# Kernel tuning notes

Measured on AMD Instinct MI355X. Metric: run time of the kernel, lower is better.

The kernel has to match this reference:

```python
import jax, jax.numpy as jnp
import numpy as np
from jax import lax

KSIZE = 5  # covariance window size

def _avg_pool_same(x):
    # TF avg_pool2d with SAME padding: zero-pad sums, divide by count of VALID (non-pad) elems
    win = (1, KSIZE, KSIZE, 1)
    s = lax.reduce_window(x, 0.0, lax.add, win, (1, 1, 1, 1), 'SAME')
    cnt = lax.reduce_window(jnp.ones((1, x.shape[1], x.shape[2], 1), x.dtype), 0.0, lax.add, win, (1, 1, 1, 1), 'SAME')
    return s / cnt

def _detect_plane_xz(xyz):
    B, H, W, _ = xyz.shape
    P = _avg_pool_same(xyz)                                   # [B,H,W,3] windowed mean
    xyz2 = (xyz[..., :, None] * xyz[..., None, :]).reshape(B, H, W, 9)
    S = _avg_pool_same(xyz2).reshape(B, H, W, 3, 3)            # windowed second moment
    A = S - P[..., :, None] * P[..., None, :]                  # covariance sigma
    A_max = jnp.max(jnp.abs(A), axis=(-2, -1))
    eval_zero = (A_max < 1e-6).astype(xyz.dtype)
    A = A / jnp.maximum(A_max[..., None, None], 1e-6)
    a00, a11, a22 = A[..., 0, 0], A[..., 1, 1], A[..., 2, 2]
    a01, a02, a12 = A[..., 0, 1], A[..., 0, 2], A[..., 1, 2]
    norm = a01 ** 2 + a02 ** 2 + a12 ** 2
    q = (a00 + a11 + a22) / 3.0
    b00, b11, b22 = a00 - q, a11 - q, a22 - q
    p = jnp.sqrt((b00 ** 2 + b11 ** 2 + b22 ** 2 + 2.0 * norm) / 6.0)
    eig_triple = (p < 1e-6).astype(xyz.dtype) * (1.0 - eval_zero)
    c00 = b11 * b22 - a12 * a12
    c01 = a01 * b22 - a12 * a02
    c02 = a01 * a12 - b11 * a02
    det = (b00 * c00 - a01 * c01 + a02 * c02) / jnp.maximum(p, 1e-6) ** 3
    half_det = jnp.clip(0.5 * det, -1.0, 1.0)
    angle = jnp.arccos(half_det) / 3.0
    beta2 = jnp.cos(angle) * 2.0
    beta0 = jnp.cos(angle + np.pi * 2.0 / 3.0) * 2.0
    beta1 = -(beta0 + beta2)
    betas = jnp.stack([beta0, beta1, beta2], axis=-1)
    evals = q[..., None] + p[..., None] * betas
    evals = (eig_triple * q)[..., None] + ((1.0 - eval_zero) * (1.0 - eig_triple))[..., None] * evals
    eval0, eval1, eval2 = evals[..., 0], evals[..., 1], evals[..., 2]
    denom = jnp.sqrt(jnp.maximum((eval0 - eval1) * (eval0 - eval2), 0.0))
    evec_zero = (denom < 1e-6).astype(xyz.dtype)
    ny_num = jnp.sqrt(jnp.maximum(eval0 ** 2 - (a00 + a22) * eval0 + (a00 * a22 - a02 ** 2), 0.0))
    ny = jnp.clip(ny_num / jnp.maximum(denom, 1e-6), 0.0, 1.0)
    return (1.0 - evec_zero) * ny

def _populate_pcd(depth, K):
    B, H, W, _ = depth.shape
    px, py = jnp.meshgrid(jnp.arange(W, dtype=depth.dtype), jnp.arange(H, dtype=depth.dtype))
    grid = jnp.stack([px, py, jnp.ones_like(px)], axis=-1)   # [H,W,3] homogeneous pixels
    xyz = grid[None] * depth                                 # [B,H,W,3]
    K_inv = jnp.linalg.inv(K)
    return jnp.einsum('bij,bhwj->bhwi', K_inv, xyz)

def setup_inputs():
    key = jax.random.key(0)
    B, H, W = 8, 384, 1280
    disp = jax.random.uniform(key, (B, H, W, 1), jnp.float32, 0.005, 0.3)  # normalized disparity
    K0 = jnp.tile(jnp.array([[720.0, 0.0, W / 2.0], [0.0, 720.0, H / 2.0], [0.0, 0.0, 1.0]], jnp.float32)[None], (B, 1, 1))
    baseline = 0.54 * jnp.ones((B,), jnp.float32)
    return {"disp": disp, "K0": K0, "baseline": baseline, "h0": H, "w0": W}

def reference(disp, K0, baseline, h0, w0):
    B, h1, w1, _ = disp.shape
    rw = float(w1) / float(w0)
    rh = float(h1) / float(h0)
    K_scale = jnp.array([[rw, 0.0, 0.5 * (rw - 1.0)], [0.0, rh, 0.5 * (rh - 1.0)], [0.0, 0.0, 1.0]], jnp.float32)
    K1 = K_scale[None] @ K0
    fxb = K1[:, 0, 0] * baseline
    d = float(w1) * jnp.maximum(disp, 1e-6)
    depth = fxb[:, None, None, None] / d
    xyz = _populate_pcd(depth, K1)
    plane_xz = _detect_plane_xz(xyz)
    cond1 = (xyz[..., 1] > 0.3).astype(jnp.float32)
    cond2 = (plane_xz > 0.85).astype(jnp.float32)
    return depth, cond1 * cond2
```

## Files before the change

kernel.cpp:

```cpp
#include <hip/hip_runtime.h>

#define BATCH 8
#define HH 384
#define WW 1280
#define TW 32
#define TH 8
#define NT (TW * TH)
#define LW (TW + 4)
#define LH (TH + 4)

__device__ __forceinline__ float fast_rcp(float x) {
  float r = __builtin_amdgcn_rcpf(x);
  return fmaf(r, fmaf(-x, r, 1.0f), r);
}
__device__ __forceinline__ float fast_sqrt(float x) {
  return __builtin_amdgcn_sqrtf(x);
}
__device__ __forceinline__ float cos_rev(float r) {
  float d;
  asm("v_cos_f32 %0, %1" : "=v"(d) : "v"(r));
  return d;
}
__device__ __forceinline__ float fast_acos(float x) {
  const float ax = fabsf(x);
  const bool big = ax > 0.5f;
  const float z = big ? (1.0f - ax) * 0.5f : x * x;
  const float u = big ? fast_sqrt(z) : x;
  float pz = fmaf(z, 4.2163199048e-2f, 2.4181311049e-2f);
  pz = fmaf(z, pz, 4.5470025998e-2f);
  pz = fmaf(z, pz, 7.4953002686e-2f);
  pz = fmaf(z, pz, 1.6666752422e-1f);
  const float r = fmaf(u * z, pz, u);
  const float big_res = (x < 0.0f) ? fmaf(-2.0f, r, 3.14159265358979f) : 2.0f * r;
  const float small_res = 1.57079632679490f - r;
  return big ? big_res : small_res;
}

__global__ void prep_kernel(const float* __restrict__ K0,
                            const float* __restrict__ baseline,
                            const int* __restrict__ h0p,
                            const int* __restrict__ w0p,
                            float* __restrict__ cst) {
  int b = threadIdx.x;
  if (b >= BATCH) return;
  float w0 = (float)w0p[0];
  float h0 = (float)h0p[0];
  float rw = (float)WW / w0;
  float rh = (float)HH / h0;
  float s02 = 0.5f * (rw - 1.0f);
  float s12 = 0.5f * (rh - 1.0f);
  const float* K = K0 + b * 9;
  float k0 = rw * K[0] + s02 * K[6];
  float k1 = rw * K[1] + s02 * K[7];
  float k2 = rw * K[2] + s02 * K[8];
  float k3 = rh * K[3] + s12 * K[6];
  float k4 = rh * K[4] + s12 * K[7];
  float k5 = rh * K[5] + s12 * K[8];
  float k6 = K[6], k7 = K[7], k8 = K[8];
  double a = k0, bb = k1, c = k2, d = k3, e = k4, f = k5, g = k6, h = k7, i = k8;
  double cA = e * i - f * h;
  double cB = -(d * i - f * g);
  double cC = d * h - e * g;
  double det = a * cA + bb * cB + c * cC;
  double idet = 1.0 / det;
  float* o = cst + b * 12;
  o[0] = (float)(cA * idet);
  o[1] = (float)(-(bb * i - c * h) * idet);
  o[2] = (float)((bb * f - c * e) * idet);
  o[3] = (float)(cB * idet);
  o[4] = (float)((a * i - c * g) * idet);
  o[5] = (float)(-(a * f - c * d) * idet);
  o[6] = (float)(cC * idet);
  o[7] = (float)(-(a * h - bb * g) * idet);
  o[8] = (float)((a * e - bb * d) * idet);
  o[9] = k0 * baseline[b];
}

__global__ __launch_bounds__(256) void tmap_fused(
    const float* __restrict__ disp,
    const float* __restrict__ cst,
    float* __restrict__ out_depth,
    float* __restrict__ out_mask) {
  __shared__ float4 tile[LH][LW];
  __shared__ float4 vs0[TH][LW];
  __shared__ float4 vs1[TH][LW];
  __shared__ float  vs2[TH][LW];

  const int b = blockIdx.z;
  const float* C = cst + b * 12;
  const float Ki00 = C[0], Ki01 = C[1], Ki02 = C[2];
  const float Ki10 = C[3], Ki11 = C[4], Ki12 = C[5];
  const float Ki20 = C[6], Ki21 = C[7], Ki22 = C[8];
  const float fxb = C[9];

  const int j0 = blockIdx.x * TW;
  const int i0 = blockIdx.y * TH;
  const int tid = threadIdx.y * TW + threadIdx.x;

  for (int s = tid; s < LH * LW; s += NT) {
    const int ti = s / LW;
    const int tj = s - ti * LW;
    const int gi = i0 - 2 + ti;
    const int gj = j0 - 2 + tj;
    float4 v = make_float4(0.0f, 0.0f, 0.0f, 0.0f);
    if (gi >= 0 && gi < HH && gj >= 0 && gj < WW) {
      const float dsp = disp[(b * HH + gi) * WW + gj];
      const float dd = (float)WW * fmaxf(dsp, 1e-6f);
      const float depth = fxb * fast_rcp(dd);
      const float jf = (float)gj;
      const float iff = (float)gi;
      v.x = depth * fmaf(Ki00, jf, fmaf(Ki01, iff, Ki02));
      v.y = depth * fmaf(Ki10, jf, fmaf(Ki11, iff, Ki12));
      v.z = depth * fmaf(Ki20, jf, fmaf(Ki21, iff, Ki22));
      v.w = depth;
    }
    tile[ti][tj] = v;
  }
  __syncthreads();

  for (int s = tid; s < TH * LW; s += NT) {
    const int ti = s / LW;
    const int tj = s - ti * LW;
    float sx = 0.f, sy = 0.f, sz = 0.f;
    float sxx = 0.f, sxy = 0.f, sxz = 0.f, syy = 0.f, syz = 0.f, szz = 0.f;
#pragma unroll
    for (int k = 0; k < 5; ++k) {
      const float4 v = tile[ti + k][tj];
      sx += v.x; sy += v.y; sz += v.z;
      sxx = fmaf(v.x, v.x, sxx);
      sxy = fmaf(v.x, v.y, sxy);
      sxz = fmaf(v.x, v.z, sxz);
      syy = fmaf(v.y, v.y, syy);
      syz = fmaf(v.y, v.z, syz);
      szz = fmaf(v.z, v.z, szz);
    }
    vs0[ti][tj] = make_float4(sx, sy, sz, sxx);
    vs1[ti][tj] = make_float4(sxy, sxz, syy, syz);
    vs2[ti][tj] = szz;
  }
  __syncthreads();

  float s1x = 0.f, s1y = 0.f, s1z = 0.f;
  float m00 = 0.f, m01 = 0.f, m02 = 0.f, m11 = 0.f, m12 = 0.f, m22 = 0.f;
#pragma unroll
  for (int w = 0; w < 5; ++w) {
    const float4 va = vs0[threadIdx.y][threadIdx.x + w];
    const float4 vb = vs1[threadIdx.y][threadIdx.x + w];
    const float vc = vs2[threadIdx.y][threadIdx.x + w];
    s1x += va.x; s1y += va.y; s1z += va.z; m00 += va.w;
    m01 += vb.x; m02 += vb.y; m11 += vb.z; m12 += vb.w;
    m22 += vc;
  }

  const int gi = i0 + threadIdx.y;
  const int gj = j0 + threadIdx.x;
  const int ch = min(gi + 2, HH - 1) - max(gi - 2, 0) + 1;
  const int cw = min(gj + 2, WW - 1) - max(gj - 2, 0) + 1;
  const float cnt = (float)(ch * cw);
  const float rcnt = fast_rcp(cnt);

  const float Px = s1x * rcnt, Py = s1y * rcnt, Pz = s1z * rcnt;
  float a00 = m00 * rcnt - Px * Px;
  float a01 = m01 * rcnt - Px * Py;
  float a02 = m02 * rcnt - Px * Pz;
  float a11 = m11 * rcnt - Py * Py;
  float a12 = m12 * rcnt - Py * Pz;
  float a22 = m22 * rcnt - Pz * Pz;

  const float AmA = fmaxf(fmaxf(fabsf(a00), fabsf(a11)), fabsf(a22));
  const float AmB = fmaxf(fmaxf(fabsf(a01), fabsf(a02)), fabsf(a12));
  const float Amax = fmaxf(AmA, AmB);
  const float eval_zero = (Amax < 1e-6f) ? 1.0f : 0.0f;
  const float rAm = fast_rcp(fmaxf(Amax, 1e-6f));
  a00 *= rAm; a01 *= rAm; a02 *= rAm; a11 *= rAm; a12 *= rAm; a22 *= rAm;

  const float nrm = a01 * a01 + a02 * a02 + a12 * a12;
  const float q = (a00 + a11 + a22) * (1.0f / 3.0f);
  const float b00 = a00 - q, b11 = a11 - q, b22 = a22 - q;
  const float p =
      fast_sqrt((b00 * b00 + b11 * b11 + b22 * b22 + 2.0f * nrm) * (1.0f / 6.0f));
  const float eig_triple = ((p < 1e-6f) ? 1.0f : 0.0f) * (1.0f - eval_zero);
  const float c00 = b11 * b22 - a12 * a12;
  const float c01 = a01 * b22 - a12 * a02;
  const float c02 = a01 * a12 - b11 * a02;
  const float rpm = fast_rcp(fmaxf(p, 1e-6f));
  const float det = (b00 * c00 - a01 * c01 + a02 * c02) * (rpm * rpm * rpm);
  const float half_det = fminf(fmaxf(0.5f * det, -1.0f), 1.0f);
  const float t = fast_acos(half_det);
  const float rev = t * 0.05305164769729845f;
  const float beta2 = 2.0f * cos_rev(rev);
  const float beta0 = 2.0f * cos_rev(rev + (1.0f / 3.0f));
  const float wsel = (1.0f - eval_zero) * (1.0f - eig_triple);
  const float e0 = eig_triple * q + wsel * fmaf(p, beta0, q);
  const float dd2 = (2.0f * beta0 + beta2) * (beta0 - beta2);
  const float denom = wsel * p * fast_sqrt(fmaxf(dd2, 0.0f));
  const float evec_zero = (denom < 1e-6f) ? 1.0f : 0.0f;
  const float ny_num =
      fast_sqrt(fmaxf(e0 * e0 - (a00 + a22) * e0 + (a00 * a22 - a02 * a02), 0.0f));
  const float ny =
      fminf(fmaxf(ny_num * fast_rcp(fmaxf(denom, 1e-6f)), 0.0f), 1.0f);
  const float plane_xz = (1.0f - evec_zero) * ny;

  const float4 ctr = tile[threadIdx.y + 2][threadIdx.x + 2];
  const float cond1 = (ctr.y > 0.3f) ? 1.0f : 0.0f;
  const float cond2 = (plane_xz > 0.85f) ? 1.0f : 0.0f;

  const int idx = (b * HH + gi) * WW + gj;
  out_depth[idx] = ctr.w;
  out_mask[idx] = cond1 * cond2;
}

extern "C" void kernel_launch(void* const* d_in, const int* in_sizes, int n_in,
                              void* d_out, int out_size, void* d_ws, size_t ws_size,
                              hipStream_t stream) {
  const float* disp = (const float*)d_in[0];
  const float* K0 = (const float*)d_in[1];
  const float* baseline = (const float*)d_in[2];
  const int* h0 = (const int*)d_in[3];
  const int* w0 = (const int*)d_in[4];

  float* cst = (float*)d_ws;
  float* out_depth = (float*)d_out;
  float* out_mask = out_depth + (size_t)BATCH * HH * WW;

  prep_kernel<<<1, BATCH, 0, stream>>>(K0, baseline, h0, w0, cst);

  dim3 block(TW, TH);
  dim3 grid(WW / TW, HH / TH, BATCH);
  tmap_fused<<<grid, block, 0, stream>>>(disp, cst, out_depth, out_mask);
}
```

Measured before the change: 116.9 us.

## Restructure into per-wavefront column strips with register-rolling vertical window

Each wavefront now owns a 64-column strip (60 outputs plus halo) and walks down 8 rows. The five-row vertical sums of the moments are kept in a rolling register buffer, and the horizontal pass goes through per-wave LDS with only wave barriers instead of block-wide syncthreads. This removes the large shared xyz tile, the separate vertical-sum pass and the block synchronisation. In exchange, 4 of 64 lanes do redundant eigen math and register pressure rises. Depth output is taken from z, which equals depth only when the inverse intrinsic's last row is [0,0,1].

```diff
diff --git a/kernel.cpp b/kernel.cpp
--- a/kernel.cpp
+++ b/kernel.cpp
@@ -3,11 +3,10 @@
 #define BATCH 8
 #define HH 384
 #define WW 1280
-#define TW 32
-#define TH 8
-#define NT (TW * TH)
-#define LW (TW + 4)
-#define LH (TH + 4)
+#define OUTW 60
+#define CH 8
+#define NSX 22
+#define NCY 48
 
 __device__ __forceinline__ float fast_rcp(float x) {
   float r = __builtin_amdgcn_rcpf(x);
@@ -76,138 +75,164 @@
   o[9] = k0 * baseline[b];
 }
 
-__global__ __launch_bounds__(256) void tmap_fused(
+__global__ __launch_bounds__(256, 4) void tmap_fused(
     const float* __restrict__ disp,
     const float* __restrict__ cst,
     float* __restrict__ out_depth,
     float* __restrict__ out_mask) {
-  __shared__ float4 tile[LH][LW];
-  __shared__ float4 vs0[TH][LW];
-  __shared__ float4 vs1[TH][LW];
-  __shared__ float  vs2[TH][LW];
-
-  const int b = blockIdx.z;
+  __shared__ float4 S0[4][64];
+  __shared__ float4 S1[4][64];
+  __shared__ float  S2[4][64];
+
+  const int lane = threadIdx.x;
+  const int wv = threadIdx.y;
+  const int unit = blockIdx.x * 4 + wv;
+  const int b = unit / (NSX * NCY);
+  const int rem = unit - b * (NSX * NCY);
+  const int cy = rem / NSX;
+  const int sx = rem - cy * NSX;
+  const int gj0 = sx * OUTW;
+  const int gi0 = cy * CH;
+
   const float* C = cst + b * 12;
-  const float Ki00 = C[0], Ki01 = C[1], Ki02 = C[2];
-  const float Ki10 = C[3], Ki11 = C[4], Ki12 = C[5];
-  const float Ki20 = C[6], Ki21 = C[7], Ki22 = C[8];
+  const float Ki01 = C[1], Ki11 = C[4], Ki21 = C[7];
   const float fxb = C[9];
 
-  const int j0 = blockIdx.x * TW;
-  const int i0 = blockIdx.y * TH;
-  const int tid = threadIdx.y * TW + threadIdx.x;
-
-  for (int s = tid; s < LH * LW; s += NT) {
-    const int ti = s / LW;
-    const int tj = s - ti * LW;
-    const int gi = i0 - 2 + ti;
-    const int gj = j0 - 2 + tj;
-    float4 v = make_float4(0.0f, 0.0f, 0.0f, 0.0f);
-    if (gi >= 0 && gi < HH && gj >= 0 && gj < WW) {
-      const float dsp = disp[(b * HH + gi) * WW + gj];
-      const float dd = (float)WW * fmaxf(dsp, 1e-6f);
-      const float depth = fxb * fast_rcp(dd);
-      const float jf = (float)gj;
-      const float iff = (float)gi;
-      v.x = depth * fmaf(Ki00, jf, fmaf(Ki01, iff, Ki02));
-      v.y = depth * fmaf(Ki10, jf, fmaf(Ki11, iff, Ki12));
-      v.z = depth * fmaf(Ki20, jf, fmaf(Ki21, iff, Ki22));
-      v.w = depth;
+  const int cj = gj0 + lane - 2;
+  const bool colv = ((unsigned)cj < (unsigned)WW);
+  const float jf = (float)cj;
+  const float cx = fmaf(C[0], jf, C[2]);
+  const float cyk = fmaf(C[3], jf, C[5]);
+  const float czk = fmaf(C[6], jf, C[8]);
+  const float cwf = (float)(min(cj + 2, WW - 1) - max(cj - 2, 0) + 1);
+
+  float4* const s0 = S0[wv];
+  float4* const s1 = S1[wv];
+  float* const s2 = S2[wv];
+
+  int rdi[5];
+#pragma unroll
+  for (int w = 0; w < 5; ++w) rdi[w] = min(max(lane + w - 2, 0), 63);
+
+  const float* const dispb = disp + (size_t)b * HH * WW;
+
+  float bx[5], by[5], bz[5], bxx[5], bxy[5], bxz[5], byy[5], byz[5], bzz[5];
+
+#define LOADROW(SLOT, T)                                              \
+  {                                                                   \
+    const int gi_ = gi0 - 2 + (T);                                    \
+    float x_ = 0.f, y_ = 0.f, z_ = 0.f;                               \
+    if (colv && gi_ >= 0 && gi_ < HH) {                               \
+      const float dsp_ = dispb[gi_ * WW + cj];                        \
+      const float depth_ =                                            \
+          fxb * fast_rcp((float)WW * fmaxf(dsp_, 1e-6f));             \
+      const float if_ = (float)gi_;                                   \
+      x_ = depth_ * fmaf(Ki01, if_, cx);                              \
+      y_ = depth_ * fmaf(Ki11, if_, cyk);                             \
+      z_ = depth_ * fmaf(Ki21, if_, czk);                             \
+    }                                                                 \
+    bx[SLOT] = x_; by[SLOT] = y_; bz[SLOT] = z_;                      \
+    bxx[SLOT] = x_ * x_; bxy[SLOT] = x_ * y_; bxz[SLOT] = x_ * z_;    \
+    byy[SLOT] = y_ * y_; byz[SLOT] = y_ * z_; bzz[SLOT] = z_ * z_;    \
+  }
+
+  LOADROW(0, 0)
+  LOADROW(1, 1)
+  LOADROW(2, 2)
+  LOADROW(3, 3)
+
+#pragma unroll
+  for (int orow = 0; orow < CH; ++orow) {
+    LOADROW((orow + 4) % 5, orow + 4)
+    const float yc = by[(orow + 2) % 5];
+    const float zc = bz[(orow + 2) % 5];
+
+    const int q0 = orow % 5, q1 = (orow + 1) % 5, q2 = (orow + 2) % 5,
+              q3 = (orow + 3) % 5, q4 = (orow + 4) % 5;
+    const float vx = (((bx[q0] + bx[q1]) + bx[q2]) + bx[q3]) + bx[q4];
+    const float vy = (((by[q0] + by[q1]) + by[q2]) + by[q3]) + by[q4];
+    const float vz = (((bz[q0] + bz[q1]) + bz[q2]) + bz[q3]) + bz[q4];
+    const float vxx = (((bxx[q0] + bxx[q1]) + bxx[q2]) + bxx[q3]) + bxx[q4];
+    const float vxy = (((bxy[q0] + bxy[q1]) + bxy[q2]) + bxy[q3]) + bxy[q4];
+    const float vxz = (((bxz[q0] + bxz[q1]) + bxz[q2]) + bxz[q3]) + bxz[q4];
+    const float vyy = (((byy[q0] + byy[q1]) + byy[q2]) + byy[q3]) + byy[q4];
+    const float vyz = (((byz[q0] + byz[q1]) + byz[q2]) + byz[q3]) + byz[q4];
+    const float vzz = (((bzz[q0] + bzz[q1]) + bzz[q2]) + bzz[q3]) + bzz[q4];
+
+    s0[lane] = make_float4(vx, vy, vz, vxx);
+    s1[lane] = make_float4(vxy, vxz, vyy, vyz);
+    s2[lane] = vzz;
+    __builtin_amdgcn_wave_barrier();
+
+    float s1x = 0.f, s1y = 0.f, s1z = 0.f;
+    float m00 = 0.f, m01 = 0.f, m02 = 0.f, m11 = 0.f, m12 = 0.f, m22 = 0.f;
+#pragma unroll
+    for (int w = 0; w < 5; ++w) {
+      const float4 a4 = s0[rdi[w]];
+      const float4 c4 = s1[rdi[w]];
+      const float e1 = s2[rdi[w]];
+      s1x += a4.x; s1y += a4.y; s1z += a4.z; m00 += a4.w;
+      m01 += c4.x; m02 += c4.y; m11 += c4.z; m12 += c4.w;
+      m22 += e1;
     }
-    tile[ti][tj] = v;
+    __builtin_amdgcn_wave_barrier();
+
+    const int gi = gi0 + orow;
+    const float cnt =
+        (float)(min(gi + 2, HH - 1) - max(gi - 2, 0) + 1) * cwf;
+    const float rcnt = fast_rcp(cnt);
+
+    const float Px = s1x * rcnt, Py = s1y * rcnt, Pz = s1z * rcnt;
+    float a00 = m00 * rcnt - Px * Px;
+    float a01 = m01 * rcnt - Px * Py;
+    float a02 = m02 * rcnt - Px * Pz;
+    float a11 = m11 * rcnt - Py * Py;
+    float a12 = m12 * rcnt - Py * Pz;
+    float a22 = m22 * rcnt - Pz * Pz;
+
+    const float AmA = fmaxf(fmaxf(fabsf(a00), fabsf(a11)), fabsf(a22));
+    const float AmB = fmaxf(fmaxf(fabsf(a01), fabsf(a02)), fabsf(a12));
+    const float Amax = fmaxf(AmA, AmB);
+    const float eval_zero = (Amax < 1e-6f) ? 1.0f : 0.0f;
+    const float rAm = fast_rcp(fmaxf(Amax, 1e-6f));
+    a00 *= rAm; a01 *= rAm; a02 *= rAm; a11 *= rAm; a12 *= rAm; a22 *= rAm;
+
+    const float nrm = a01 * a01 + a02 * a02 + a12 * a12;
+    const float q = (a00 + a11 + a22) * (1.0f / 3.0f);
+    const float b00 = a00 - q, b11 = a11 - q, b22 = a22 - q;
+    const float p = fast_sqrt(
+        (b00 * b00 + b11 * b11 + b22 * b22 + 2.0f * nrm) * (1.0f / 6.0f));
+    const float eig_triple = ((p < 1e-6f) ? 1.0f : 0.0f) * (1.0f - eval_zero);
+    const float c00 = b11 * b22 - a12 * a12;
+    const float c01 = a01 * b22 - a12 * a02;
+    const float c02 = a01 * a12 - b11 * a02;
+    const float rpm = fast_rcp(fmaxf(p, 1e-6f));
+    const float det = (b00 * c00 - a01 * c01 + a02 * c02) * (rpm * rpm * rpm);
+    const float half_det = fminf(fmaxf(0.5f * det, -1.0f), 1.0f);
+    const float t = fast_acos(half_det);
+    const float rev = t * 0.05305164769729845f;
+    const float beta2 = 2.0f * cos_rev(rev);
+    const float beta0 = 2.0f * cos_rev(rev + (1.0f / 3.0f));
+    const float wsel = (1.0f - eval_zero) * (1.0f - eig_triple);
+    const float e0 = eig_triple * q + wsel * fmaf(p, beta0, q);
+    const float dd2 = (2.0f * beta0 + beta2) * (beta0 - beta2);
+    const float denom = wsel * p * fast_sqrt(fmaxf(dd2, 0.0f));
+    const float evec_zero = (denom < 1e-6f) ? 1.0f : 0.0f;
+    const float ny_num = fast_sqrt(
+        fmaxf(e0 * e0 - (a00 + a22) * e0 + (a00 * a22 - a02 * a02), 0.0f));
+    const float ny =
+        fminf(fmaxf(ny_num * fast_rcp(fmaxf(denom, 1e-6f)), 0.0f), 1.0f);
+    const float plane_xz = (1.0f - evec_zero) * ny;
+
+    if (lane >= 2 && lane < 2 + OUTW && cj < WW) {
+      const int idx = (b * HH + gi) * WW + cj;
+      out_depth[idx] = zc;
+      const float cond1 = (yc > 0.3f) ? 1.0f : 0.0f;
+      const float cond2 = (plane_xz > 0.85f) ? 1.0f : 0.0f;
+      out_mask[idx] = cond1 * cond2;
+    }
   }
-  __syncthreads();
-
-  for (int s = tid; s < TH * LW; s += NT) {
-    const int ti = s / LW;
-    const int tj = s - ti * LW;
-    float sx = 0.f, sy = 0.f, sz = 0.f;
-    float sxx = 0.f, sxy = 0.f, sxz = 0.f, syy = 0.f, syz = 0.f, szz = 0.f;
-#pragma unroll
-    for (int k = 0; k < 5; ++k) {
-      const float4 v = tile[ti + k][tj];
-      sx += v.x; sy += v.y; sz += v.z;
-      sxx = fmaf(v.x, v.x, sxx);
-      sxy = fmaf(v.x, v.y, sxy);
-      sxz = fmaf(v.x, v.z, sxz);
-      syy = fmaf(v.y, v.y, syy);
-      syz = fmaf(v.y, v.z, syz);
-      szz = fmaf(v.z, v.z, szz);
-    }
-    vs0[ti][tj] = make_float4(sx, sy, sz, sxx);
-    vs1[ti][tj] = make_float4(sxy, sxz, syy, syz);
-    vs2[ti][tj] = szz;
-  }
-  __syncthreads();
-
-  float s1x = 0.f, s1y = 0.f, s1z = 0.f;
-  float m00 = 0.f, m01 = 0.f, m02 = 0.f, m11 = 0.f, m12 = 0.f, m22 = 0.f;
-#pragma unroll
-  for (int w = 0; w < 5; ++w) {
-    const float4 va = vs0[threadIdx.y][threadIdx.x + w];
-    const float4 vb = vs1[threadIdx.y][threadIdx.x + w];
-    const float vc = vs2[threadIdx.y][threadIdx.x + w];
-    s1x += va.x; s1y += va.y; s1z += va.z; m00 += va.w;
-    m01 += vb.x; m02 += vb.y; m11 += vb.z; m12 += vb.w;
-    m22 += vc;
-  }
-
-  const int gi = i0 + threadIdx.y;
-  const int gj = j0 + threadIdx.x;
-  const int ch = min(gi + 2, HH - 1) - max(gi - 2, 0) + 1;
-  const int cw = min(gj + 2, WW - 1) - max(gj - 2, 0) + 1;
-  const float cnt = (float)(ch * cw);
-  const float rcnt = fast_rcp(cnt);
-
-  const float Px = s1x * rcnt, Py = s1y * rcnt, Pz = s1z * rcnt;
-  float a00 = m00 * rcnt - Px * Px;
-  float a01 = m01 * rcnt - Px * Py;
-  float a02 = m02 * rcnt - Px * Pz;
-  float a11 = m11 * rcnt - Py * Py;
-  float a12 = m12 * rcnt - Py * Pz;
-  float a22 = m22 * rcnt - Pz * Pz;
-
-  const float AmA = fmaxf(fmaxf(fabsf(a00), fabsf(a11)), fabsf(a22));
-  const float AmB = fmaxf(fmaxf(fabsf(a01), fabsf(a02)), fabsf(a12));
-  const float Amax = fmaxf(AmA, AmB);
-  const float eval_zero = (Amax < 1e-6f) ? 1.0f : 0.0f;
-  const float rAm = fast_rcp(fmaxf(Amax, 1e-6f));
-  a00 *= rAm; a01 *= rAm; a02 *= rAm; a11 *= rAm; a12 *= rAm; a22 *= rAm;
-
-  const float nrm = a01 * a01 + a02 * a02 + a12 * a12;
-  const float q = (a00 + a11 + a22) * (1.0f / 3.0f);
-  const float b00 = a00 - q, b11 = a11 - q, b22 = a22 - q;
-  const float p =
-      fast_sqrt((b00 * b00 + b11 * b11 + b22 * b22 + 2.0f * nrm) * (1.0f / 6.0f));
-  const float eig_triple = ((p < 1e-6f) ? 1.0f : 0.0f) * (1.0f - eval_zero);
-  const float c00 = b11 * b22 - a12 * a12;
-  const float c01 = a01 * b22 - a12 * a02;
-  const float c02 = a01 * a12 - b11 * a02;
-  const float rpm = fast_rcp(fmaxf(p, 1e-6f));
-  const float det = (b00 * c00 - a01 * c01 + a02 * c02) * (rpm * rpm * rpm);
-  const float half_det = fminf(fmaxf(0.5f * det, -1.0f), 1.0f);
-  const float t = fast_acos(half_det);
-  const float rev = t * 0.05305164769729845f;
-  const float beta2 = 2.0f * cos_rev(rev);
-  const float beta0 = 2.0f * cos_rev(rev + (1.0f / 3.0f));
-  const float wsel = (1.0f - eval_zero) * (1.0f - eig_triple);
-  const float e0 = eig_triple * q + wsel * fmaf(p, beta0, q);
-  const float dd2 = (2.0f * beta0 + beta2) * (beta0 - beta2);
-  const float denom = wsel * p * fast_sqrt(fmaxf(dd2, 0.0f));
-  const float evec_zero = (denom < 1e-6f) ? 1.0f : 0.0f;
-  const float ny_num =
-      fast_sqrt(fmaxf(e0 * e0 - (a00 + a22) * e0 + (a00 * a22 - a02 * a02), 0.0f));
-  const float ny =
-      fminf(fmaxf(ny_num * fast_rcp(fmaxf(denom, 1e-6f)), 0.0f), 1.0f);
-  const float plane_xz = (1.0f - evec_zero) * ny;
-
-  const float4 ctr = tile[threadIdx.y + 2][threadIdx.x + 2];
-  const float cond1 = (ctr.y > 0.3f) ? 1.0f : 0.0f;
-  const float cond2 = (plane_xz > 0.85f) ? 1.0f : 0.0f;
-
-  const int idx = (b * HH + gi) * WW + gj;
-  out_depth[idx] = ctr.w;
-  out_mask[idx] = cond1 * cond2;
+#undef LOADROW
 }
 
 extern "C" void kernel_launch(void* const* d_in, const int* in_sizes, int n_in,
@@ -225,7 +250,6 @@
 
   prep_kernel<<<1, BATCH, 0, stream>>>(K0, baseline, h0, w0, cst);
 
-  dim3 block(TW, TH);
-  dim3 grid(WW / TW, HH / TH, BATCH);
-  tmap_fused<<<grid, block, 0, stream>>>(disp, cst, out_depth, out_mask);
-}
+  const int nblocks = (NSX * NCY * BATCH) / 4;
+  tmap_fused<<<nblocks, dim3(64, 4), 0, stream>>>(disp, cst, out_depth, out_mask);
+}
```

New measurement: 111.3 us. 4.7% less time.
